# Optimization experiments

Hardware: AMD Instinct MI355X
Metric: run time of the kernel (lower is better)

The kernel has to match this reference:

```python
import math
import jax, jax.numpy as jnp
import numpy as np

NHID = 1024
HEADS = 16
SEQ = 1024
BATCH = 8


def setup_inputs() -> dict:
    key = jax.random.key(0)
    ks = jax.random.split(key, 12)
    s = 0.02
    inp = {
        "query": jax.random.normal(ks[0], (SEQ, BATCH, NHID), jnp.float32),
        "key": jax.random.normal(ks[1], (SEQ, BATCH, NHID), jnp.float32),
        "value": jax.random.normal(ks[2], (SEQ, BATCH, NHID), jnp.float32),
        "qs_p": jax.random.normal(ks[3], (1, 1, NHID), jnp.float32) * s,
        "ks_p": jax.random.normal(ks[4], (1, 1, NHID), jnp.float32) * s,
        "vs_p": jax.random.normal(ks[5], (1, 1, NHID), jnp.float32) * s,
        "Wq": jax.random.normal(ks[6], (NHID, NHID), jnp.float32) * s,
        "bq": jax.random.normal(ks[7], (NHID,), jnp.float32) * s,
        "Wzf": jax.random.normal(ks[8], (2 * NHID, NHID), jnp.float32) * s,
        "bzf": jax.random.normal(ks[9], (2 * NHID,), jnp.float32) * s,
    }
    # additive causal mask, viewed as (1,1,S,S) and added to scores
    causal = jnp.triu(jnp.ones((SEQ, SEQ), jnp.float32), k=1) * (-1e9)
    inp["attn_mask"] = causal
    return inp


def reference(query, key, value, qs_p, ks_p, vs_p, Wq, bq, Wzf, bzf, attn_mask):
    nhid = NHID
    heads = HEADS
    dim = nhid // heads

    # sigmoid gates on Q/K/V scales
    qs = jax.nn.sigmoid(qs_p)              # (1,1,nhid)
    ks_g = jax.nn.sigmoid(ks_p)
    vs_in = jax.nn.sigmoid(vs_p)

    # QRNNLayer(window=1, output_gate=False) on single-step vs:
    # z = tanh(Wz vs + bz), f = sigmoid(Wf vs + bf), h = f * z (h0 = 0)
    zf = jnp.einsum('abn,mn->abm', vs_in, Wzf) + bzf   # (1,1,2*nhid)
    z = jnp.tanh(zf[..., :nhid])
    f = jax.nn.sigmoid(zf[..., nhid:])
    vs = f * z                                          # (1,1,nhid)

    # q projection (k,v have no Linear with defaults)
    q_lin = jnp.einsum('sbn,mn->sbm', query, Wq) + bq

    q = qs * q_lin       # (S,B,nhid)
    k = ks_g * key
    v = vs * value

    # seq-first -> batch-first, split heads
    def split_heads(t):
        t = t.transpose(1, 0, 2)                         # (B,S,nhid)
        B, S, _ = t.shape
        return t.reshape(B, S, heads, dim).transpose(0, 2, 1, 3)  # (B,H,S,d)

    qh, kh, vh = split_heads(q), split_heads(k), split_heads(v)

    scores = jnp.einsum('bhqd,bhkd->bhqk', qh, kh) / math.sqrt(dim)
    scores = scores + attn_mask[None, None]              # (B,H,S,S)
    weights = jax.nn.softmax(scores, axis=-1)
    mix = jnp.einsum('bhqk,bhkd->bhqd', weights, vh)     # (B,H,S,d)

    B = mix.shape[0]
    mix = mix.transpose(0, 2, 1, 3).reshape(B, -1, nhid)  # (B,S,nhid)
    mix = mix.transpose(1, 0, 2)                          # (S,B,nhid) seq-first
    return mix, weights
```

## Files before the change

### kernel.cpp

```cpp
#include <hip/hip_runtime.h>

typedef unsigned short u16;
typedef unsigned int   u32;
typedef float  f32x4  __attribute__((ext_vector_type(4)));
typedef short  bf16x8 __attribute__((ext_vector_type(8)));
typedef unsigned short u16x8 __attribute__((ext_vector_type(8)));
typedef unsigned short u16x4 __attribute__((ext_vector_type(4)));
typedef unsigned int   u32x2 __attribute__((ext_vector_type(2)));

#define DEV __device__ __forceinline__

constexpr int S  = 1024;
constexpr int BB = 8;
constexpr int NH = 1024;
constexpr int H  = 16;

DEV u16 f2bf(float f) {
  union { float f; unsigned u; } v{f};
  unsigned r = v.u + 0x7FFFu + ((v.u >> 16) & 1u);
  return (u16)(r >> 16);
}
DEV float sigm(float x) { return 1.0f / (1.0f + __expf(-x)); }
DEV float exp2a(float x) { float r; asm("v_exp_f32 %0, %1" : "=v"(r) : "v"(x)); return r; }

DEV void gload_lds16(const void* g, void* l) {
  __builtin_amdgcn_global_load_lds(
      (const __attribute__((address_space(1))) unsigned int*)g,
      (__attribute__((address_space(3))) unsigned int*)l, 16, 0, 0);
}

DEV f32x4 ntload4(const float* p) {
  return __builtin_nontemporal_load((const f32x4*)p);
}
DEV void ntstore4(f32x4 v, float* p) {
  __builtin_nontemporal_store(v, (f32x4*)p);
}

constexpr float SC = 0.18033688f;

__global__ __launch_bounds__(256) void k_prep(
    const float* __restrict__ query, const float* __restrict__ key,
    const float* __restrict__ value, const float* __restrict__ qs_p,
    const float* __restrict__ ks_p,  const float* __restrict__ vs_p,
    const float* __restrict__ Wq,   const float* __restrict__ bq,
    const float* __restrict__ Wzf,  const float* __restrict__ bzf,
    u16* __restrict__ qx, u16* __restrict__ kout, u16* __restrict__ vout,
    float* __restrict__ vsg, float* __restrict__ bq2, u16* __restrict__ wq_bf)
{
  __shared__ float tile[64][65];
  if (blockIdx.x >= 4096) {
    int m = (blockIdx.x - 4096) * 4 + (threadIdx.x >> 6);
    int l = threadIdx.x & 63;
    const float* wz = Wzf + (size_t)m * NH;
    const float* wf = Wzf + (size_t)(m + NH) * NH;
    int base = l * 16;
    float za = 0.f, fa = 0.f;
#pragma unroll
    for (int i = 0; i < 16; i += 4) {
      f32x4 vp  = *(const f32x4*)(vs_p + base + i);
      f32x4 wzv = *(const f32x4*)(wz + base + i);
      f32x4 wfv = *(const f32x4*)(wf + base + i);
      float v0 = sigm(vp.x), v1 = sigm(vp.y), v2 = sigm(vp.z), v3 = sigm(vp.w);
      za += v0 * wzv.x + v1 * wzv.y + v2 * wzv.z + v3 * wzv.w;
      fa += v0 * wfv.x + v1 * wfv.y + v2 * wfv.z + v3 * wfv.w;
    }
#pragma unroll
    for (int off = 1; off < 64; off <<= 1) {
      za += __shfl_xor(za, off);
      fa += __shfl_xor(fa, off);
    }
    float z   = tanhf(za + bzf[m]);
    float f   = sigm(fa + bzf[m + NH]);
    float qsm = sigm(qs_p[m]);
    if (l == 0) {
      vsg[m] = f * z;
      bq2[m] = qsm * bq[m] * SC;
    }
    float qss = qsm * SC;
    const float* wqr = Wq + (size_t)m * NH;
    u16* dst = wq_bf + (size_t)m * NH + base;
#pragma unroll
    for (int i = 0; i < 16; i += 4) {
      f32x4 wv = *(const f32x4*)(wqr + base + i);
      u16x4 o;
      o[0] = f2bf(qss * wv.x); o[1] = f2bf(qss * wv.y);
      o[2] = f2bf(qss * wv.z); o[3] = f2bf(qss * wv.w);
      *(u16x4*)(dst + i) = o;
    }
    return;
  }
  size_t idx = ((size_t)blockIdx.x * 256 + threadIdx.x) * 8;
  {
    f32x4 a = ntload4(query + idx);
    f32x4 b = ntload4(query + idx + 4);
    u16x8 o;
    o[0] = f2bf(a.x); o[1] = f2bf(a.y); o[2] = f2bf(a.z); o[3] = f2bf(a.w);
    o[4] = f2bf(b.x); o[5] = f2bf(b.y); o[6] = f2bf(b.z); o[7] = f2bf(b.w);
    *(u16x8*)(qx + idx) = o;
  }
  {
    int n0 = (int)(idx & 1023);
    int b  = (int)((idx >> 10) & 7);
    int s  = (int)(idx >> 13);
    f32x4 a  = ntload4(key + idx);
    f32x4 c  = ntload4(key + idx + 4);
    f32x4 k0 = *(const f32x4*)(ks_p + n0);
    f32x4 k1 = *(const f32x4*)(ks_p + n0 + 4);
    int h = n0 >> 6, d0 = n0 & 63;
    u16* dst = kout + (((size_t)(b * H + h) * S + s) * 64 + d0);
    u16x8 o;
    o[0] = f2bf(a.x * sigm(k0.x)); o[1] = f2bf(a.y * sigm(k0.y));
    o[2] = f2bf(a.z * sigm(k0.z)); o[3] = f2bf(a.w * sigm(k0.w));
    o[4] = f2bf(c.x * sigm(k1.x)); o[5] = f2bf(c.y * sigm(k1.y));
    o[6] = f2bf(c.z * sigm(k1.z)); o[7] = f2bf(c.w * sigm(k1.w));
    *(u16x8*)dst = o;
  }
  if (blockIdx.x < 2048) {
    int bh = blockIdx.x >> 4, kt = blockIdx.x & 15;
    int b = bh >> 4, h = bh & 15;
    int t = threadIdx.x;
    int sp = t >> 2, c0 = (t & 3) * 16;
    const float* src = value + ((size_t)(kt * 64 + sp) * (BB * NH) + b * NH + h * 64 + c0);
#pragma unroll
    for (int i = 0; i < 16; i += 4) {
      f32x4 v = ntload4(src + i);
      tile[sp][c0 + i + 0] = v.x;
      tile[sp][c0 + i + 1] = v.y;
      tile[sp][c0 + i + 2] = v.z;
      tile[sp][c0 + i + 3] = v.w;
    }
    __syncthreads();
    int d = t >> 2, s0 = (t & 3) * 16;
    u16* dst = vout + (((size_t)bh * 16 + kt) * 64 + d) * 64 + s0;
    u16x8 o0, o1;
#pragma unroll
    for (int i = 0; i < 8; ++i) o0[i] = f2bf(tile[s0 + i][d]);
#pragma unroll
    for (int i = 0; i < 8; ++i) o1[i] = f2bf(tile[s0 + 8 + i][d]);
    *(u16x8*)dst       = o0;
    *(u16x8*)(dst + 8) = o1;
  }
}

__global__ __launch_bounds__(256, 4) void k_attn(
    const u16* __restrict__ qx, const u16* __restrict__ wqb,
    const float* __restrict__ bq2, const u16* __restrict__ kws,
    const u16* __restrict__ vtw, const float* __restrict__ vsg,
    float* __restrict__ mix, float* __restrict__ wout)
{
  __shared__ __align__(16) char smem[40960];
  int bid = blockIdx.x;
  int b = bid & 7;
  int idx = bid >> 3;
  int h = idx & 15, t = 15 - (idx >> 4);
  int bh = b * 16 + h;
  int tid = threadIdx.x, w = tid >> 6, l = tid & 63;
  int g = l >> 4, lq = l & 15;
  int q0 = t * 64;
  int myq = q0 + 16 * w + lq;
  int jmax = t;
  float* wbase = wout + (size_t)bh * S * S;
  int srow = l >> 3, sblk = l & 7;

  u16* As = (u16*)smem;
  u16* Bs = (u16*)(smem + 16384);
  u16* Qs = (u16*)smem;
  u16* K1 = (u16*)(smem + 8192);
  u16* K2 = (u16*)(smem + 8192);
  u16* V2 = (u16*)(smem + 24576);

  {
    auto stageA = [&](int kt, int buf) {
#pragma unroll
      for (int ii = 0; ii < 2; ++ii) {
        int row = w * 16 + ii * 8 + srow;
        int blk = sblk ^ (row & 7);
        gload_lds16(qx + ((size_t)((q0 + row) * 8 + b) * 1024 + kt * 64 + blk * 8),
                    &As[buf * 4096 + (w * 2 + ii) * 512]);
      }
    };
    auto stageB = [&](int kt, int buf) {
#pragma unroll
      for (int ii = 0; ii < 2; ++ii) {
        int row = w * 16 + ii * 8 + srow;
        int blk = sblk ^ (row & 7);
        gload_lds16(wqb + ((size_t)(h * 64 + row) * 1024 + kt * 64 + blk * 8),
                    &Bs[buf * 4096 + (w * 2 + ii) * 512]);
      }
    };
    f32x4 acc[4];
    f32x4 zero4 = {0.f, 0.f, 0.f, 0.f};
#pragma unroll
    for (int fj = 0; fj < 4; ++fj) acc[fj] = zero4;
    stageA(0, 0); stageB(0, 0);
    for (int kt = 0; kt < 16; ++kt) {
      asm volatile("s_waitcnt vmcnt(0)" ::: "memory");
      __builtin_amdgcn_sched_barrier(0);
      __builtin_amdgcn_s_barrier();
      __builtin_amdgcn_sched_barrier(0);
      if (kt < 15) { stageA(kt + 1, (kt + 1) & 1); stageB(kt + 1, (kt + 1) & 1); }
      __builtin_amdgcn_sched_barrier(0);
      int ab = (kt & 1) * 4096, bb = (kt & 1) * 4096;
      __builtin_amdgcn_s_setprio(1);
#pragma unroll
      for (int kk = 0; kk < 2; ++kk) {
        int ar = 16 * w + lq;
        bf16x8 av = *(const bf16x8*)&As[ab + ar * 64 + ((((kk << 2) + g) ^ (ar & 7)) << 3)];
#pragma unroll
        for (int fj = 0; fj < 4; ++fj) {
          int br = fj * 16 + lq;
          bf16x8 bv = *(const bf16x8*)&Bs[bb + br * 64 + ((((kk << 2) + g) ^ (br & 7)) << 3)];
          acc[fj] = __builtin_amdgcn_mfma_f32_16x16x32_bf16(av, bv, acc[fj], 0, 0, 0);
        }
      }
      __builtin_amdgcn_s_setprio(0);
    }
    float bq4[4];
#pragma unroll
    for (int fj = 0; fj < 4; ++fj) bq4[fj] = bq2[h * 64 + fj * 16 + lq];
#pragma unroll
    for (int fj = 0; fj < 4; ++fj) {
      int d = fj * 16 + lq;
#pragma unroll
      for (int r = 0; r < 4; ++r) {
        int qrow = 16 * w + (g << 2) + r;
        Qs[qrow * 64 + (((fj * 2 + (d >> 3 & 1)) ^ (qrow & 7)) << 3) + (d & 7)] =
            f2bf(acc[fj][r] + bq4[fj]);
      }
    }
    __syncthreads();
  }
  bf16x8 qa[2];
#pragma unroll
  for (int kk = 0; kk < 2; ++kk) {
    int qr = 16 * w + lq;
    qa[kk] = *(const bf16x8*)&Qs[qr * 64 + ((((kk << 2) + g) ^ (qr & 7)) << 3)];
  }
  asm volatile("s_waitcnt lgkmcnt(0)" ::: "memory");
  __builtin_amdgcn_sched_barrier(0);
  __builtin_amdgcn_s_barrier();

  auto stageK1 = [&](int j, int buf) {
#pragma unroll
    for (int ii = 0; ii < 2; ++ii) {
      int row = w * 16 + ii * 8 + srow;
      int blk = sblk ^ (row & 7);
      gload_lds16(kws + ((size_t)bh * S + j * 64 + row) * 64 + blk * 8,
                  &K1[buf * 4096 + (w * 2 + ii) * 512]);
    }
  };

  float lsum = 0.f;
  {
    stageK1(0, 0);
    if (jmax >= 1) stageK1(1, 1);
    auto qkTile = [&](int j) {
      int jb = (j & 3) * 4096;
      f32x4 sacc[4];
      f32x4 zero4 = {0.f, 0.f, 0.f, 0.f};
#pragma unroll
      for (int fj = 0; fj < 4; ++fj) sacc[fj] = zero4;
      __builtin_amdgcn_s_setprio(1);
#pragma unroll
      for (int kk = 0; kk < 2; ++kk)
#pragma unroll
        for (int fj = 0; fj < 4; ++fj) {
          int kr = fj * 16 + lq;
          bf16x8 kb = *(const bf16x8*)&K1[jb + kr * 64 + ((((kk << 2) + g) ^ (kr & 7)) << 3)];
          sacc[fj] = __builtin_amdgcn_mfma_f32_16x16x32_bf16(kb, qa[kk], sacc[fj], 0, 0, 0);
        }
      __builtin_amdgcn_s_setprio(0);
      if (j < jmax) {
#pragma unroll
        for (int fj = 0; fj < 4; ++fj)
#pragma unroll
          for (int r = 0; r < 4; ++r) lsum += exp2a(sacc[fj][r]);
      } else {
#pragma unroll
        for (int fj = 0; fj < 4; ++fj)
#pragma unroll
          for (int r = 0; r < 4; ++r) {
            int ki = j * 64 + fj * 16 + 4 * g + r;
            if (ki <= myq) lsum += exp2a(sacc[fj][r]);
          }
      }
    };
    int nslot = (jmax + 2) >> 1;
    for (int s = 0; s < nslot; ++s) {
      int j0 = 2 * s, j1 = 2 * s + 1;
      asm volatile("s_waitcnt vmcnt(0)" ::: "memory");
      __builtin_amdgcn_sched_barrier(0);
      __builtin_amdgcn_s_barrier();
      __builtin_amdgcn_sched_barrier(0);
      if (j0 + 2 <= jmax) stageK1(j0 + 2, (j0 + 2) & 3);
      if (j0 + 3 <= jmax) stageK1(j0 + 3, (j0 + 3) & 3);
      __builtin_amdgcn_sched_barrier(0);
      qkTile(j0);
      if (j1 <= jmax) qkTile(j1);
    }
  }
  lsum += __shfl_xor(lsum, 16);
  lsum += __shfl_xor(lsum, 32);
  float invl = 1.0f / lsum;

  __builtin_amdgcn_s_barrier();

  auto stageK2 = [&](int j, int buf) {
#pragma unroll
    for (int ii = 0; ii < 2; ++ii) {
      int row = w * 16 + ii * 8 + srow;
      int blk = sblk ^ (row & 7);
      gload_lds16(kws + ((size_t)bh * S + j * 64 + row) * 64 + blk * 8,
                  &K2[buf * 4096 + (w * 2 + ii) * 512]);
    }
  };
  auto stageV2 = [&](int j, int buf) {
#pragma unroll
    for (int ii = 0; ii < 2; ++ii) {
      int row = w * 16 + ii * 8 + srow;
      int blk = sblk ^ (row & 7);
      gload_lds16(vtw + (((size_t)bh * 16 + j) * 64 + row) * 64 + blk * 8,
                  &V2[buf * 4096 + (w * 2 + ii) * 512]);
    }
  };
  stageK2(0, 0); stageV2(0, 0);
  f32x4 oacc[4];
  {
    f32x4 zero4 = {0.f, 0.f, 0.f, 0.f};
#pragma unroll
    for (int db = 0; db < 4; ++db) oacc[db] = zero4;
  }
  char* pb = smem + w * 2048;
  int pswz = (lq & 7) * 16;
  for (int j = 0; j <= jmax; ++j) {
    if (j == 0) asm volatile("s_waitcnt vmcnt(0)" ::: "memory");
    else        asm volatile("s_waitcnt vmcnt(4)" ::: "memory");
    __builtin_amdgcn_sched_barrier(0);
    __builtin_amdgcn_s_barrier();
    __builtin_amdgcn_sched_barrier(0);
    if (j < jmax) { stageK2(j + 1, (j + 1) & 1); stageV2(j + 1, (j + 1) & 1); }
    __builtin_amdgcn_sched_barrier(0);
    int kbase = (j & 1) * 4096;
    f32x4 sacc[4];
    f32x4 zero4 = {0.f, 0.f, 0.f, 0.f};
#pragma unroll
    for (int fj = 0; fj < 4; ++fj) sacc[fj] = zero4;
    __builtin_amdgcn_s_setprio(1);
#pragma unroll
    for (int kk = 0; kk < 2; ++kk)
#pragma unroll
      for (int fj = 0; fj < 4; ++fj) {
        int kr = fj * 16 + lq;
        bf16x8 kb = *(const bf16x8*)&K2[kbase + kr * 64 + ((((kk << 2) + g) ^ (kr & 7)) << 3)];
        sacc[fj] = __builtin_amdgcn_mfma_f32_16x16x32_bf16(kb, qa[kk], sacc[fj], 0, 0, 0);
      }
    __builtin_amdgcn_s_setprio(0);
    bool diag = (j == jmax);
    float p0[4], p1[4], p2[4], p3[4];
#pragma unroll
    for (int fj = 0; fj < 4; ++fj) {
      float* pp = fj == 0 ? p0 : fj == 1 ? p1 : fj == 2 ? p2 : p3;
#pragma unroll
      for (int r = 0; r < 4; ++r) {
        float e = exp2a(sacc[fj][r]) * invl;
        if (diag) {
          int ki = j * 64 + fj * 16 + 4 * g + r;
          if (ki > myq) e = 0.f;
        }
        pp[r] = e;
      }
    }
#pragma unroll
    for (int fj = 0; fj < 4; ++fj) {
      float* pp = fj == 0 ? p0 : fj == 1 ? p1 : fj == 2 ? p2 : p3;
      u32 w0, w1;
      asm("v_cvt_pk_bf16_f32 %0, %1, %2" : "=v"(w0) : "v"(pp[0]), "v"(pp[1]));
      asm("v_cvt_pk_bf16_f32 %0, %1, %2" : "=v"(w1) : "v"(pp[2]), "v"(pp[3]));
      u32x2 wv = {w0, w1};
      *(u32x2*)(pb + lq * 128 + ((fj * 32 + g * 8) ^ pswz)) = wv;
    }
#pragma unroll
    for (int fj = 0; fj < 4; ++fj) {
      float* pp = fj == 0 ? p0 : fj == 1 ? p1 : fj == 2 ? p2 : p3;
      f32x4 f4 = {pp[0], pp[1], pp[2], pp[3]};
      *(f32x4*)(wbase + (size_t)myq * S + j * 64 + fj * 16 + g * 4) = f4;
    }
    asm volatile("s_waitcnt lgkmcnt(0)" ::: "memory");
    __builtin_amdgcn_sched_barrier(0);
    __builtin_amdgcn_s_setprio(1);
#pragma unroll
    for (int kk = 0; kk < 2; ++kk) {
      bf16x8 pa = *(const bf16x8*)(pb + lq * 128 + ((kk * 64 + g * 16) ^ pswz));
#pragma unroll
      for (int db = 0; db < 4; ++db) {
        int d = db * 16 + lq;
        bf16x8 vb = *(const bf16x8*)&V2[(j & 1) * 4096 + d * 64 + ((((kk << 2) + g) ^ (d & 7)) << 3)];
        oacc[db] = __builtin_amdgcn_mfma_f32_16x16x32_bf16(pa, vb, oacc[db], 0, 0, 0);
      }
    }
    __builtin_amdgcn_s_setprio(0);
  }

  float vs4[4];
#pragma unroll
  for (int db = 0; db < 4; ++db) vs4[db] = vsg[h * 64 + db * 16 + lq];
#pragma unroll
  for (int db = 0; db < 4; ++db) {
#pragma unroll
    for (int r = 0; r < 4; ++r) {
      int qi = q0 + 16 * w + 4 * g + r;
      mix[(size_t)(qi * BB + b) * NH + h * 64 + db * 16 + lq] = oacc[db][r] * vs4[db];
    }
  }

  {
    f32x4 z4 = {0.f, 0.f, 0.f, 0.f};
    int cstart = (jmax + 1) * 64;
    for (int lr = 0; lr < 16; ++lr) {
      float* rowp = wbase + (size_t)(q0 + 16 * w + lr) * S;
      for (int c = cstart + l * 4; c < S; c += 256)
        ntstore4(z4, rowp + c);
    }
  }
}

extern "C" void kernel_launch(void* const* d_in, const int* in_sizes, int n_in,
                              void* d_out, int out_size, void* d_ws, size_t ws_size,
                              hipStream_t stream) {
  (void)in_sizes; (void)n_in; (void)out_size; (void)ws_size;
  const float* query = (const float*)d_in[0];
  const float* key   = (const float*)d_in[1];
  const float* value = (const float*)d_in[2];
  const float* qs_p  = (const float*)d_in[3];
  const float* ks_p  = (const float*)d_in[4];
  const float* vs_p  = (const float*)d_in[5];
  const float* Wq    = (const float*)d_in[6];
  const float* bq    = (const float*)d_in[7];
  const float* Wzf   = (const float*)d_in[8];
  const float* bzf   = (const float*)d_in[9];

  char* ws = (char*)d_ws;
  float* vsg  = (float*)(ws + 0x1000);
  float* bq2  = (float*)(ws + 0x2000);
  u16* wq_bf  = (u16*)(ws + 0x4000);
  u16* qx_bf  = (u16*)(ws + 0x204000);
  u16* k_ws   = (u16*)(ws + 0x1204000);
  u16* vt_ws  = (u16*)(ws + 0x2204000);

  float* mix  = (float*)d_out;
  float* wout = mix + (size_t)S * BB * NH;

  k_prep<<<4352, 256, 0, stream>>>(query, key, value, qs_p, ks_p, vs_p,
                                   Wq, bq, Wzf, bzf,
                                   qx_bf, k_ws, vt_ws, vsg, bq2, wq_bf);
  k_attn<<<2048, 256, 0, stream>>>(qx_bf, wq_bf, bq2, k_ws, vt_ws, vsg,
                                   mix, wout);
}
```

Baseline: 186.0 us.

## Replace LDS P round-trip with ds_bpermute shuffles and shrink LDS for occupancy

The softmax probabilities are now converted to bf16 and rearranged into the MFMA A-operand layout with ds_bpermute register shuffles, instead of being written to an LDS scratch area and read back. This frees the per-wave P buffer, so shared memory drops from 40KB to 32KB and the launch bound asks for 5 blocks per CU. It removes the LDS write, the lgkmcnt wait and the read on the inner loop, but adds 16 bpermutes and selects per iteration, and register pressure may rise under the tighter occupancy target.

```diff
diff --git a/kernel.cpp b/kernel.cpp
--- a/kernel.cpp
+++ b/kernel.cpp
@@ -7,6 +7,7 @@
 typedef unsigned short u16x8 __attribute__((ext_vector_type(8)));
 typedef unsigned short u16x4 __attribute__((ext_vector_type(4)));
 typedef unsigned int   u32x2 __attribute__((ext_vector_type(2)));
+typedef unsigned int   u32x4 __attribute__((ext_vector_type(4)));
 
 #define DEV __device__ __forceinline__
 
@@ -142,13 +143,13 @@
   }
 }
 
-__global__ __launch_bounds__(256, 4) void k_attn(
+__global__ __launch_bounds__(256, 5) void k_attn(
     const u16* __restrict__ qx, const u16* __restrict__ wqb,
     const float* __restrict__ bq2, const u16* __restrict__ kws,
     const u16* __restrict__ vtw, const float* __restrict__ vsg,
     float* __restrict__ mix, float* __restrict__ wout)
 {
-  __shared__ __align__(16) char smem[40960];
+  __shared__ __align__(16) char smem[32768];
   int bid = blockIdx.x;
   int b = bid & 7;
   int idx = bid >> 3;
@@ -165,9 +166,9 @@
   u16* As = (u16*)smem;
   u16* Bs = (u16*)(smem + 16384);
   u16* Qs = (u16*)smem;
-  u16* K1 = (u16*)(smem + 8192);
-  u16* K2 = (u16*)(smem + 8192);
-  u16* V2 = (u16*)(smem + 24576);
+  u16* K1 = (u16*)smem;
+  u16* K2 = (u16*)smem;
+  u16* V2 = (u16*)(smem + 16384);
 
   {
     auto stageA = [&](int kt, int buf) {
@@ -330,8 +331,8 @@
 #pragma unroll
     for (int db = 0; db < 4; ++db) oacc[db] = zero4;
   }
-  char* pb = smem + w * 2048;
-  int pswz = (lq & 7) * 16;
+  int srcA = ((32 * (g & 1) + lq) << 2);
+  int srcB = srcA + 64;
   for (int j = 0; j <= jmax; ++j) {
     if (j == 0) asm volatile("s_waitcnt vmcnt(0)" ::: "memory");
     else        asm volatile("s_waitcnt vmcnt(4)" ::: "memory");
@@ -356,10 +357,8 @@
       }
     __builtin_amdgcn_s_setprio(0);
     bool diag = (j == jmax);
-    float p0[4], p1[4], p2[4], p3[4];
 #pragma unroll
     for (int fj = 0; fj < 4; ++fj) {
-      float* pp = fj == 0 ? p0 : fj == 1 ? p1 : fj == 2 ? p2 : p3;
 #pragma unroll
       for (int r = 0; r < 4; ++r) {
         float e = exp2a(sacc[fj][r]) * invl;
@@ -367,30 +366,49 @@
           int ki = j * 64 + fj * 16 + 4 * g + r;
           if (ki > myq) e = 0.f;
         }
-        pp[r] = e;
-      }
-    }
-#pragma unroll
-    for (int fj = 0; fj < 4; ++fj) {
-      float* pp = fj == 0 ? p0 : fj == 1 ? p1 : fj == 2 ? p2 : p3;
-      u32 w0, w1;
-      asm("v_cvt_pk_bf16_f32 %0, %1, %2" : "=v"(w0) : "v"(pp[0]), "v"(pp[1]));
-      asm("v_cvt_pk_bf16_f32 %0, %1, %2" : "=v"(w1) : "v"(pp[2]), "v"(pp[3]));
-      u32x2 wv = {w0, w1};
-      *(u32x2*)(pb + lq * 128 + ((fj * 32 + g * 8) ^ pswz)) = wv;
-    }
-#pragma unroll
-    for (int fj = 0; fj < 4; ++fj) {
-      float* pp = fj == 0 ? p0 : fj == 1 ? p1 : fj == 2 ? p2 : p3;
-      f32x4 f4 = {pp[0], pp[1], pp[2], pp[3]};
-      *(f32x4*)(wbase + (size_t)myq * S + j * 64 + fj * 16 + g * 4) = f4;
-    }
-    asm volatile("s_waitcnt lgkmcnt(0)" ::: "memory");
-    __builtin_amdgcn_sched_barrier(0);
+        sacc[fj][r] = e;
+      }
+    }
+#pragma unroll
+    for (int fj = 0; fj < 4; ++fj)
+      *(f32x4*)(wbase + (size_t)myq * S + j * 64 + fj * 16 + g * 4) = sacc[fj];
+    u32 W0, W1, W2, W3, W4, W5, W6, W7;
+    asm("v_cvt_pk_bf16_f32 %0, %1, %2" : "=v"(W0) : "v"(sacc[0][0]), "v"(sacc[0][1]));
+    asm("v_cvt_pk_bf16_f32 %0, %1, %2" : "=v"(W1) : "v"(sacc[0][2]), "v"(sacc[0][3]));
+    asm("v_cvt_pk_bf16_f32 %0, %1, %2" : "=v"(W2) : "v"(sacc[1][0]), "v"(sacc[1][1]));
+    asm("v_cvt_pk_bf16_f32 %0, %1, %2" : "=v"(W3) : "v"(sacc[1][2]), "v"(sacc[1][3]));
+    asm("v_cvt_pk_bf16_f32 %0, %1, %2" : "=v"(W4) : "v"(sacc[2][0]), "v"(sacc[2][1]));
+    asm("v_cvt_pk_bf16_f32 %0, %1, %2" : "=v"(W5) : "v"(sacc[2][2]), "v"(sacc[2][3]));
+    asm("v_cvt_pk_bf16_f32 %0, %1, %2" : "=v"(W6) : "v"(sacc[3][0]), "v"(sacc[3][1]));
+    asm("v_cvt_pk_bf16_f32 %0, %1, %2" : "=v"(W7) : "v"(sacc[3][2]), "v"(sacc[3][3]));
+    u32 a0 = __builtin_amdgcn_ds_bpermute(srcA, (int)W0);
+    u32 a1 = __builtin_amdgcn_ds_bpermute(srcA, (int)W1);
+    u32 a2 = __builtin_amdgcn_ds_bpermute(srcA, (int)W2);
+    u32 a3 = __builtin_amdgcn_ds_bpermute(srcA, (int)W3);
+    u32 a4 = __builtin_amdgcn_ds_bpermute(srcA, (int)W4);
+    u32 a5 = __builtin_amdgcn_ds_bpermute(srcA, (int)W5);
+    u32 a6 = __builtin_amdgcn_ds_bpermute(srcA, (int)W6);
+    u32 a7 = __builtin_amdgcn_ds_bpermute(srcA, (int)W7);
+    u32 b0 = __builtin_amdgcn_ds_bpermute(srcB, (int)W0);
+    u32 b1 = __builtin_amdgcn_ds_bpermute(srcB, (int)W1);
+    u32 b2 = __builtin_amdgcn_ds_bpermute(srcB, (int)W2);
+    u32 b3 = __builtin_amdgcn_ds_bpermute(srcB, (int)W3);
+    u32 b4 = __builtin_amdgcn_ds_bpermute(srcB, (int)W4);
+    u32 b5 = __builtin_amdgcn_ds_bpermute(srcB, (int)W5);
+    u32 b6 = __builtin_amdgcn_ds_bpermute(srcB, (int)W6);
+    u32 b7 = __builtin_amdgcn_ds_bpermute(srcB, (int)W7);
+    bool hi = (g >> 1) != 0;
+    u32x4 paw0, paw1;
+    paw0[0] = hi ? a2 : a0;  paw0[1] = hi ? a3 : a1;
+    paw0[2] = hi ? b2 : b0;  paw0[3] = hi ? b3 : b1;
+    paw1[0] = hi ? a6 : a4;  paw1[1] = hi ? a7 : a5;
+    paw1[2] = hi ? b6 : b4;  paw1[3] = hi ? b7 : b5;
+    bf16x8 pa0 = __builtin_bit_cast(bf16x8, paw0);
+    bf16x8 pa1 = __builtin_bit_cast(bf16x8, paw1);
     __builtin_amdgcn_s_setprio(1);
 #pragma unroll
     for (int kk = 0; kk < 2; ++kk) {
-      bf16x8 pa = *(const bf16x8*)(pb + lq * 128 + ((kk * 64 + g * 16) ^ pswz));
+      bf16x8 pa = kk ? pa1 : pa0;
 #pragma unroll
       for (int db = 0; db < 4; ++db) {
         int d = db * 16 + lq;
```

Measured after the change: 184.8 us. Within noise of the previous version (-0.7%).
